# Kernel tuning notes

Measured on AMD Instinct MI355X. Metric: run time of the kernel, lower is better.

Reference implementation:

```python
import jax, jax.numpy as jnp
import numpy as np

B, S, H = 2, 2048, 2048
E, K = 8, 2            # num_local_experts, num_experts_per_tok
I, IS = 1024, 4096     # expert / shared-expert intermediate dims


def setup_inputs() -> dict:
    key = jax.random.key(0)
    ks = jax.random.split(key, 8)
    w = lambda k, shp: jax.random.normal(k, shp, dtype=jnp.float32) * 0.02
    return {
        "hidden_states": jax.random.normal(ks[0], (B, S, H), dtype=jnp.float32),
        "router_w": w(ks[1], (E, H)),
        "gate_w": w(ks[2], (E, I, H)),
        "up_w": w(ks[3], (E, I, H)),
        "down_w": w(ks[4], (E, H, I)),
        "shared_gate_w": w(ks[5], (IS, H)),
        "shared_up_w": w(ks[6], (IS, H)),
        "shared_down_w": w(ks[7], (H, IS)),
    }


def reference(hidden_states, router_w, gate_w, up_w, down_w,
              shared_gate_w, shared_up_w, shared_down_w):
    x = hidden_states  # [B,S,H]
    b, s, h = x.shape

    # Router: logits over experts, top-k, sigmoid of top values (computed in fp32)
    router_logits = jnp.einsum('bsh,eh->bse', x, router_w)           # [B,S,E]
    top_vals, top_idx = jax.lax.top_k(router_logits, K)              # [B,S,K]
    scores = jax.nn.sigmoid(top_vals.astype(jnp.float32)).astype(x.dtype)

    # Per-token per-expert input scale (each expert appears at most once in top-k)
    onehot = jax.nn.one_hot(top_idx, E, dtype=x.dtype)               # [B,S,K,E]
    scale = jnp.einsum('bsk,bske->bse', scores, onehot)              # [B,S,E]

    # Routed experts: scale is applied to the INPUT of each expert (as in the torch code).
    # With bias-free gated MLP, zero-scaled (unrouted) tokens produce exact zeros,
    # so the dense formulation matches the sparse gather/scatter exactly.
    xs = x.reshape(-1, h)                                            # [T,H]
    sc = scale.reshape(-1, E)                                        # [T,E]
    xe = xs[:, None, :] * sc[:, :, None]                             # [T,E,H]
    g = jnp.einsum('teh,eih->tei', xe, gate_w)                       # [T,E,I]
    u = jnp.einsum('teh,eih->tei', xe, up_w)                         # [T,E,I]
    hmid = jax.nn.silu(g) * u
    routed = jnp.einsum('tei,ehi->th', hmid, down_w).reshape(b, s, h)

    # Shared expert (dense gated MLP over all tokens)
    sg = jnp.einsum('bsh,ih->bsi', x, shared_gate_w)
    su = jnp.einsum('bsh,ih->bsi', x, shared_up_w)
    shared = jnp.einsum('bsi,hi->bsh', jax.nn.silu(sg) * su, shared_down_w)

    return routed + shared, router_logits
```

## Files before the change

kernel.cpp:

```cpp
#include <hip/hip_runtime.h>
#include <hip/hip_bf16.h>
#include <cstdint>
#include <cstddef>

typedef __bf16 bf16x8 __attribute__((ext_vector_type(8)));
typedef float  f32x4  __attribute__((ext_vector_type(4)));

static constexpr int TOK  = 4096;
static constexpr int H    = 2048;
static constexpr int E    = 8;
static constexpr int IDIM = 1024;
static constexpr int ISD  = 4096;
static constexpr int MAXTILES = 72;
static constexpr int MAXROWS  = MAXTILES * 128;


__device__ __forceinline__ void gll16(const void* g, void* l) {
  __builtin_amdgcn_global_load_lds((const __attribute__((address_space(1))) void*)g,
                                   (__attribute__((address_space(3))) void*)l, 16, 0, 0);
}

__device__ __forceinline__ unsigned short f2bf(float f) {
  unsigned int u = __float_as_uint(f);
  u = (u + 0x7fffu + ((u >> 16) & 1u)) >> 16;
  return (unsigned short)u;
}

__global__ __launch_bounds__(256) void detect_kernel(const unsigned int* __restrict__ x,
                                                     int* __restrict__ meta) {
  __shared__ int sh[256];
  const int tid = threadIdx.x;
  int c = 0;
  for (int i = tid; i < 1024; i += 256) {
    const unsigned int e = (x[i] >> 7) & 0xFFu;
    c += (e >= 100u && e <= 150u) ? 1 : 0;
  }
  sh[tid] = c;
  if (tid >= 4 && tid < 24) meta[tid] = 0;
  __syncthreads();
  if (tid == 0) {
    int s = 0;
    for (int i = 0; i < 256; ++i) s += sh[i];
    meta[0] = (s > 512) ? 1 : 0;
  }
}

__global__ __launch_bounds__(256) void convert_all_kernel(
    const float* __restrict__ s0, const float* __restrict__ s1,
    const float* __restrict__ s2, const float* __restrict__ s3,
    const float* __restrict__ s4, const float* __restrict__ s5,
    const float* __restrict__ s6, const float* __restrict__ s7,
    unsigned short* __restrict__ d0, unsigned short* __restrict__ d1,
    unsigned short* __restrict__ d2, unsigned short* __restrict__ d3,
    unsigned short* __restrict__ d4, unsigned short* __restrict__ d5,
    unsigned short* __restrict__ d6, unsigned short* __restrict__ d7,
    const int* __restrict__ flag)
{
  if (*flag) return;
  const int stride = gridDim.x * 256;
  const int base = blockIdx.x * 256 + threadIdx.x;
  auto go = [&](const float* s, unsigned short* d, int n4) {
    for (int i = base; i < n4; i += stride) {
      const float4 v = ((const float4*)s)[i];
      ushort4 o;
      o.x = f2bf(v.x); o.y = f2bf(v.y); o.z = f2bf(v.z); o.w = f2bf(v.w);
      ((ushort4*)d)[i] = o;
    }
  };
  go(s0, d0, (TOK * H) / 4);
  go(s1, d1, (E * H) / 4);
  go(s2, d2, (E * IDIM * H) / 4);
  go(s3, d3, (E * IDIM * H) / 4);
  go(s4, d4, (E * H * IDIM) / 4);
  go(s5, d5, (ISD * H) / 4);
  go(s6, d6, (ISD * H) / 4);
  go(s7, d7, (ISD * H) / 4);
}

__global__ __launch_bounds__(256) void router_kernel(
    const void* __restrict__ x_, const void* __restrict__ rw_,
    void* __restrict__ out, float* __restrict__ scale,
    int* __restrict__ meta, int* __restrict__ topk)
{
  const int bfmode = meta[0];
  const int t   = blockIdx.x;
  const int tid = threadIdx.x;
  const int l   = tid & 63, w = tid >> 6;
  const int off = tid * 8;

  float xs[8];
  if (bfmode) {
    bf16x8 v = *(const bf16x8*)((const unsigned short*)x_ + (size_t)t * H + off);
#pragma unroll
    for (int j = 0; j < 8; ++j) xs[j] = (float)v[j];
  } else {
    const float* xr = (const float*)x_ + (size_t)t * H + off;
    const float4 a = *(const float4*)xr;
    const float4 b = *(const float4*)(xr + 4);
    xs[0]=a.x; xs[1]=a.y; xs[2]=a.z; xs[3]=a.w; xs[4]=b.x; xs[5]=b.y; xs[6]=b.z; xs[7]=b.w;
  }

  float p[E];
#pragma unroll
  for (int e = 0; e < E; ++e) {
    float wv[8];
    if (bfmode) {
      bf16x8 v = *(const bf16x8*)((const unsigned short*)rw_ + (size_t)e * H + off);
#pragma unroll
      for (int j = 0; j < 8; ++j) wv[j] = (float)v[j];
    } else {
      const float* wr = (const float*)rw_ + (size_t)e * H + off;
      const float4 a = *(const float4*)wr;
      const float4 b = *(const float4*)(wr + 4);
      wv[0]=a.x; wv[1]=a.y; wv[2]=a.z; wv[3]=a.w; wv[4]=b.x; wv[5]=b.y; wv[6]=b.z; wv[7]=b.w;
    }
    float s = 0.f;
#pragma unroll
    for (int j = 0; j < 8; ++j) s = fmaf(xs[j], wv[j], s);
    p[e] = s;
  }
#pragma unroll
  for (int e = 0; e < E; ++e)
    for (int o = 32; o > 0; o >>= 1) p[e] += __shfl_down(p[e], o);

  __shared__ float red[E][4];
  __shared__ float lg[E];
  __shared__ float sres[2];
  __shared__ int   ires[2];
  if (l == 0) {
#pragma unroll
    for (int e = 0; e < E; ++e) red[e][w] = p[e];
  }
  __syncthreads();
  if (tid < E) {
    const float v = red[tid][0] + red[tid][1] + red[tid][2] + red[tid][3];
    lg[tid] = v;
    const size_t oi = (size_t)TOK * H + (size_t)t * E + tid;
    if (bfmode) ((unsigned short*)out)[oi] = f2bf(v);
    else        ((float*)out)[oi] = v;
  }
  __syncthreads();
  if (tid == 0) {
    int i0 = 0; float v0 = lg[0];
    for (int e = 1; e < E; ++e) if (lg[e] > v0) { v0 = lg[e]; i0 = e; }
    int i1 = -1; float v1 = 0.f; bool init = false;
    for (int e = 0; e < E; ++e) {
      if (e == i0) continue;
      if (!init || lg[e] > v1) { v1 = lg[e]; i1 = e; init = true; }
    }
    sres[0] = 1.f / (1.f + expf(-v0)); ires[0] = i0;
    sres[1] = 1.f / (1.f + expf(-v1)); ires[1] = i1;
    topk[2 * t + 0] = i0;
    topk[2 * t + 1] = i1;
    atomicAdd(&meta[4 + i0], 1);
    atomicAdd(&meta[4 + i1], 1);
  }
  __syncthreads();
  if (tid < E) {
    float s = 0.f;
    if (tid == ires[0]) s = sres[0];
    else if (tid == ires[1]) s = sres[1];
    scale[(size_t)t * E + tid] = s;
  }
}

__global__ __launch_bounds__(256) void scan_kernel(int* __restrict__ meta,
                                                   int* __restrict__ list) {
  const int tid = threadIdx.x;
  if (tid == 0) {
    int s = 0, nt = 0;
    for (int e = 0; e < E; ++e) {
      meta[24 + e] = s;
      const int cnt = meta[4 + e];
      const int tiles = (cnt + 127) >> 7;
      for (int i = 0; i < tiles; ++i) {
        meta[64 + nt]  = e;
        meta[136 + nt] = s + i * 128;
        ++nt;
      }
      s += tiles << 7;
    }
    meta[32] = s;
    meta[20] = nt;
  }
  for (int i = tid; i < MAXROWS; i += 256) list[i] = 0;
}

__global__ __launch_bounds__(256) void scatter_kernel(int* __restrict__ meta,
                                                      const int* __restrict__ topk,
                                                      int* __restrict__ list,
                                                      int* __restrict__ tokpos) {
  const int t = blockIdx.x * 256 + threadIdx.x;
  if (t >= TOK) return;
#pragma unroll
  for (int k = 0; k < 2; ++k) {
    const int e = topk[2 * t + k];
    const int p = atomicAdd(&meta[12 + e], 1);
    const int g = meta[24 + e] + p;
    list[g] = t;
    tokpos[2 * t + k] = g;
  }
}

#define GU_BAR_   __builtin_amdgcn_s_barrier()
#define GU_LGKM0_ { asm volatile("s_waitcnt lgkmcnt(0)" ::: "memory"); \
                    __builtin_amdgcn_sched_barrier(0); }
#define GU_VM4_   asm volatile("s_waitcnt vmcnt(4)" ::: "memory")
#define GU_VM0_   asm volatile("s_waitcnt vmcnt(0)" ::: "memory")

#define LDA_(p, mh) { _Pragma("unroll") for (int q2 = 0; q2 < 4; ++q2) { \
  _Pragma("unroll") for (int ks = 0; ks < 2; ++ks) { \
    const int row_ = 32 * (4 * (mh) + q2) + 16 * wm + lm; \
    a[q2][ks] = *(const bf16x8*)&ldsA[(p) * 16384 + row_ * 64 + \
                                      (((ks * 4 + quad) ^ (lm & 7)) * 8)]; } } }

#define LDB_(p, nh) { _Pragma("unroll") for (int nt2 = 0; nt2 < 2; ++nt2) { \
  _Pragma("unroll") for (int ks = 0; ks < 2; ++ks) { \
    const int row_ = 16 * (wn + 4 * (2 * (nh) + nt2)) + lm; \
    bb[nh][nt2][ks] = *(const bf16x8*)&ldsB[(p) * 16384 + row_ * 64 + \
                                            (((ks * 4 + quad) ^ (lm & 7)) * 8)]; } } }

#define MFMA_(mh, nh) { __builtin_amdgcn_s_setprio(1); \
  _Pragma("unroll") for (int q2 = 0; q2 < 4; ++q2) \
  _Pragma("unroll") for (int nt2 = 0; nt2 < 2; ++nt2) \
  _Pragma("unroll") for (int ks = 0; ks < 2; ++ks) \
    acc[4 * (mh) + q2][2 * (nh) + nt2] = __builtin_amdgcn_mfma_f32_16x16x32_bf16( \
      a[q2][ks], bb[nh][nt2][ks], acc[4 * (mh) + q2][2 * (nh) + nt2], 0, 0, 0); \
  __builtin_amdgcn_s_setprio(0); }

__global__ __launch_bounds__(512, 2) void gateup_shared_kernel(
    const void* __restrict__ xo_,  const unsigned short* __restrict__ cx,
    const void* __restrict__ sgo_, const unsigned short* __restrict__ csgw,
    const void* __restrict__ suo_, const unsigned short* __restrict__ csuw,
    unsigned short* __restrict__ hmid_sh, const int* __restrict__ meta)
{
  extern __shared__ unsigned short lds[];
  unsigned short* ldsA = lds;
  unsigned short* ldsB = lds + 32768;

  const int bfmode = meta[0];
  const unsigned short* x  = bfmode ? (const unsigned short*)xo_  : cx;
  const unsigned short* gw = bfmode ? (const unsigned short*)sgo_ : csgw;
  const unsigned short* uw = bfmode ? (const unsigned short*)suo_ : csuw;

  const int tid = threadIdx.x;
  const int l = tid & 63, w = tid >> 6;
  const int wm = w >> 2, wn = w & 3;
  const int quad = l >> 4, lm = l & 15;
  const int m0 = blockIdx.x * 256;
  const int jb = blockIdx.y * 128;

  const unsigned short* gB = gw + (size_t)jb * H;
  const unsigned short* uB = uw + (size_t)jb * H;

  const int sr0 = tid >> 3,         sc0 = tid & 7;
  const int sr1 = (tid + 512) >> 3, sc1 = (tid + 512) & 7;
  const int scc0 = sc0 ^ (sr0 & 7), scc1 = sc1 ^ (sr1 & 7);
  const int sd0 = tid * 8, sd1 = (tid + 512) * 8;

  auto stA = [&](int kt, int half) {
    unsigned short* d = ldsA + (kt & 1) * 16384 + half * 8192;
    const unsigned short* s = x + (size_t)(m0 + half * 128) * H + kt * 64;
    gll16(s + (size_t)sr0 * H + scc0 * 8, d + sd0);
    gll16(s + (size_t)sr1 * H + scc1 * 8, d + sd1);
  };
  auto stB = [&](int kt, int half) {
    unsigned short* d = ldsB + (kt & 1) * 16384 + half * 8192;
    const unsigned short* s = (half ? uB : gB) + kt * 64;
    gll16(s + (size_t)sr0 * H + scc0 * 8, d + sd0);
    gll16(s + (size_t)sr1 * H + scc1 * 8, d + sd1);
  };

  f32x4 acc[8][4] = {};
  bf16x8 a[4][2];
  bf16x8 bb[2][2][2];

  stA(0, 0); stB(0, 0); stB(0, 1); stA(0, 1);
  stB(1, 1); stA(1, 1);
  GU_VM4_; GU_BAR_;

  for (int i = 0; i < (H / 128) - 1; ++i) {
    const int t0 = 2 * i, t1 = 2 * i + 1;
    LDA_(0, 0); LDB_(0, 0); stA(t1, 0);
    GU_BAR_; GU_LGKM0_; MFMA_(0, 0); GU_BAR_;
    LDB_(0, 1); stB(t1, 0);
    GU_BAR_; GU_LGKM0_; MFMA_(0, 1); GU_BAR_;
    LDA_(0, 1); stA(t0 + 2, 0);
    GU_BAR_; GU_LGKM0_; MFMA_(1, 1); GU_BAR_;
    stB(t0 + 2, 0); GU_VM4_;
    GU_BAR_; GU_LGKM0_; MFMA_(1, 0); GU_BAR_;
    LDA_(1, 0); LDB_(1, 0); stB(t0 + 2, 1);
    GU_BAR_; GU_LGKM0_; MFMA_(0, 0); GU_BAR_;
    LDB_(1, 1); stA(t0 + 2, 1);
    GU_BAR_; GU_LGKM0_; MFMA_(0, 1); GU_BAR_;
    LDA_(1, 1); stB(t1 + 2, 1);
    GU_BAR_; GU_LGKM0_; MFMA_(1, 1); GU_BAR_;
    stA(t1 + 2, 1); GU_VM4_;
    GU_BAR_; GU_LGKM0_; MFMA_(1, 0); GU_BAR_;
  }

  {
    const int t1 = H / 64 - 1;
    LDA_(0, 0); LDB_(0, 0); stA(t1, 0);
    GU_BAR_; GU_LGKM0_; MFMA_(0, 0); GU_BAR_;
    LDB_(0, 1); stB(t1, 0);
    GU_BAR_; GU_LGKM0_; MFMA_(0, 1); GU_BAR_;
    LDA_(0, 1);
    GU_BAR_; GU_LGKM0_; MFMA_(1, 1); GU_BAR_;
    GU_VM0_;
    GU_BAR_; GU_LGKM0_; MFMA_(1, 0); GU_BAR_;
    LDA_(1, 0); LDB_(1, 0);
    GU_BAR_; GU_LGKM0_; MFMA_(0, 0); GU_BAR_;
    LDB_(1, 1);
    GU_BAR_; GU_LGKM0_; MFMA_(0, 1); GU_BAR_;
    LDA_(1, 1);
    GU_BAR_; GU_LGKM0_; MFMA_(1, 1); GU_BAR_;
    MFMA_(1, 0);
  }

#pragma unroll
  for (int mt = 0; mt < 8; ++mt) {
    const int trow = m0 + 32 * mt + 16 * wm + quad * 4;
#pragma unroll
    for (int ntp = 0; ntp < 2; ++ntp) {
      const int col = jb + wn * 16 + ntp * 64 + lm;
#pragma unroll
      for (int rr = 0; rr < 4; ++rr) {
        const float g = acc[mt][ntp][rr];
        const float u = acc[mt][ntp + 2][rr];
        const float hm = (g / (1.f + expf(-g))) * u;
        hmid_sh[(size_t)(trow + rr) * ISD + col] = f2bf(hm);
      }
    }
  }
}

__global__ __launch_bounds__(256) void gateup_routed_kernel(
    const void* __restrict__ xo_,  const unsigned short* __restrict__ cx,
    const void* __restrict__ gwo_, const unsigned short* __restrict__ cgw,
    const void* __restrict__ uwo_, const unsigned short* __restrict__ cuw,
    const float* __restrict__ scale, const int* __restrict__ list,
    unsigned short* __restrict__ hmid_r, const int* __restrict__ meta)
{
  if ((int)blockIdx.x >= meta[20]) return;
  const int bfmode = meta[0];
  const unsigned short* x      = bfmode ? (const unsigned short*)xo_  : cx;
  const unsigned short* gate_w = bfmode ? (const unsigned short*)gwo_ : cgw;
  const unsigned short* up_w   = bfmode ? (const unsigned short*)uwo_ : cuw;

  __shared__ __attribute__((aligned(16))) unsigned short As[128 * 64];
  __shared__ __attribute__((aligned(16))) unsigned short Bgs[64 * 64];
  __shared__ __attribute__((aligned(16))) unsigned short Bus[64 * 64];

  const int tid = threadIdx.x;
  const int l = tid & 63, w = tid >> 6;
  const int e    = meta[64 + blockIdx.x];
  const int base = meta[136 + blockIdx.x];
  const int jj   = blockIdx.y * 64;

  const unsigned short* gB = gate_w + ((size_t)e * IDIM + jj) * H;
  const unsigned short* uB = up_w   + ((size_t)e * IDIM + jj) * H;

  int tok[4];
#pragma unroll
  for (int j = 0; j < 4; ++j) tok[j] = list[base + ((j * 256 + tid) >> 3)];

  f32x4 accg[4][2] = {};
  f32x4 accu[4][2] = {};
  const int wm = (w >> 1) * 64;
  const int wn = (w & 1) * 32;
  const int quad = l >> 4, lm = l & 15;

  for (int k0 = 0; k0 < H; k0 += 64) {
#pragma unroll
    for (int j = 0; j < 4; ++j) {
      const int g = j * 256 + tid;
      const int r = g >> 3, c = g & 7;
      const int cc = c ^ (r & 7);
      gll16(x + (size_t)tok[j] * H + k0 + cc * 8, &As[g * 8]);
    }
#pragma unroll
    for (int j = 0; j < 2; ++j) {
      const int g = j * 256 + tid;
      const int r = g >> 3, c = g & 7;
      const int cc = c ^ (r & 7);
      gll16(gB + (size_t)r * H + k0 + cc * 8, &Bgs[g * 8]);
      gll16(uB + (size_t)r * H + k0 + cc * 8, &Bus[g * 8]);
    }
    __syncthreads();
#pragma unroll
    for (int ks = 0; ks < 64; ks += 32) {
      const int kc  = (ks >> 3) + quad;
      const int csw = (kc ^ (lm & 7)) * 8;
      bf16x8 a[4], bg[2], bu[2];
#pragma unroll
      for (int mt = 0; mt < 4; ++mt)
        a[mt] = *(const bf16x8*)&As[(wm + mt * 16 + lm) * 64 + csw];
#pragma unroll
      for (int nt = 0; nt < 2; ++nt) {
        bg[nt] = *(const bf16x8*)&Bgs[(wn + nt * 16 + lm) * 64 + csw];
        bu[nt] = *(const bf16x8*)&Bus[(wn + nt * 16 + lm) * 64 + csw];
      }
#pragma unroll
      for (int mt = 0; mt < 4; ++mt)
#pragma unroll
        for (int nt = 0; nt < 2; ++nt) {
          accg[mt][nt] = __builtin_amdgcn_mfma_f32_16x16x32_bf16(a[mt], bg[nt], accg[mt][nt], 0, 0, 0);
          accu[mt][nt] = __builtin_amdgcn_mfma_f32_16x16x32_bf16(a[mt], bu[nt], accu[mt][nt], 0, 0, 0);
        }
    }
    __syncthreads();
  }

#pragma unroll
  for (int mt = 0; mt < 4; ++mt) {
#pragma unroll
    for (int r = 0; r < 4; ++r) {
      const int row  = wm + mt * 16 + quad * 4 + r;
      const int gpos = base + row;
      const int token = list[gpos];
      const float s = scale[(size_t)token * E + e];
#pragma unroll
      for (int nt = 0; nt < 2; ++nt) {
        const int j = jj + wn + nt * 16 + lm;
        const float g = accg[mt][nt][r] * s;
        const float u = accu[mt][nt][r] * s;
        const float hm = (g / (1.f + expf(-g))) * u;
        hmid_r[(size_t)gpos * IDIM + j] = f2bf(hm);
      }
    }
  }
}

__global__ __launch_bounds__(256) void down_routed_kernel(
    const unsigned short* __restrict__ hmid_r,
    const void* __restrict__ dwo_, const unsigned short* __restrict__ cdw,
    float* __restrict__ dbuf, const int* __restrict__ meta)
{
  if ((int)blockIdx.y >= meta[20]) return;
  const int bfmode = meta[0];
  const unsigned short* down_w = bfmode ? (const unsigned short*)dwo_ : cdw;

  __shared__ __attribute__((aligned(16))) unsigned short As[128 * 64];
  __shared__ __attribute__((aligned(16))) unsigned short Bs[128 * 64];

  const int tid = threadIdx.x;
  const int l = tid & 63, w = tid >> 6;
  const int e    = meta[64 + blockIdx.y];
  const int base = meta[136 + blockIdx.y];
  const int n0 = blockIdx.x * 128;

  const unsigned short* Bbase = down_w + ((size_t)e * H + n0) * IDIM;

  f32x4 acc[4][4] = {};
  const int wm = (w >> 1) * 64;
  const int wn = (w & 1) * 64;
  const int quad = l >> 4, lm = l & 15;

  for (int k0 = 0; k0 < IDIM; k0 += 64) {
#pragma unroll
    for (int j = 0; j < 4; ++j) {
      const int g = j * 256 + tid;
      const int r = g >> 3, c = g & 7;
      const int cc = c ^ (r & 7);
      gll16(hmid_r + (size_t)(base + r) * IDIM + k0 + cc * 8, &As[g * 8]);
    }
#pragma unroll
    for (int j = 0; j < 4; ++j) {
      const int g = j * 256 + tid;
      const int r = g >> 3, c = g & 7;
      const int cc = c ^ (r & 7);
      gll16(Bbase + (size_t)r * IDIM + k0 + cc * 8, &Bs[g * 8]);
    }
    __syncthreads();
#pragma unroll
    for (int ks = 0; ks < 64; ks += 32) {
      const int kc  = (ks >> 3) + quad;
      const int csw = (kc ^ (lm & 7)) * 8;
      bf16x8 a[4], b[4];
#pragma unroll
      for (int mt = 0; mt < 4; ++mt)
        a[mt] = *(const bf16x8*)&As[(wm + mt * 16 + lm) * 64 + csw];
#pragma unroll
      for (int nt = 0; nt < 4; ++nt)
        b[nt] = *(const bf16x8*)&Bs[(wn + nt * 16 + lm) * 64 + csw];
#pragma unroll
      for (int mt = 0; mt < 4; ++mt)
#pragma unroll
        for (int nt = 0; nt < 4; ++nt)
          acc[mt][nt] = __builtin_amdgcn_mfma_f32_16x16x32_bf16(a[mt], b[nt], acc[mt][nt], 0, 0, 0);
    }
    __syncthreads();
  }

#pragma unroll
  for (int mt = 0; mt < 4; ++mt)
#pragma unroll
    for (int nt = 0; nt < 4; ++nt)
#pragma unroll
      for (int r = 0; r < 4; ++r) {
        const int row = wm + mt * 16 + quad * 4 + r;
        const int n   = n0 + wn + nt * 16 + lm;
        dbuf[(size_t)(base + row) * H + n] = acc[mt][nt][r];
      }
}

__global__ __launch_bounds__(256) void down_shared_kernel(
    const unsigned short* __restrict__ hmid_sh,
    const void* __restrict__ sdwo_, const unsigned short* __restrict__ csdw,
    const float* __restrict__ dbuf, const int* __restrict__ tokpos,
    void* __restrict__ out, const int* __restrict__ meta)
{
  const int bfmode = meta[0];
  const unsigned short* sdown_w = bfmode ? (const unsigned short*)sdwo_ : csdw;

  __shared__ __attribute__((aligned(16))) unsigned short As[128 * 64];
  __shared__ __attribute__((aligned(16))) unsigned short Bs[128 * 64];

  const int tid = threadIdx.x;
  const int l = tid & 63, w = tid >> 6;
  const int m0 = blockIdx.y * 128;
  const int n0 = blockIdx.x * 128;

  f32x4 acc[4][4] = {};
  const int wm = (w >> 1) * 64;
  const int wn = (w & 1) * 64;
  const int quad = l >> 4, lm = l & 15;

  for (int k0 = 0; k0 < ISD; k0 += 64) {
#pragma unroll
    for (int j = 0; j < 4; ++j) {
      const int g = j * 256 + tid;
      const int r = g >> 3, c = g & 7;
      const int cc = c ^ (r & 7);
      gll16(hmid_sh + (size_t)(m0 + r) * ISD + k0 + cc * 8, &As[g * 8]);
    }
#pragma unroll
    for (int j = 0; j < 4; ++j) {
      const int g = j * 256 + tid;
      const int r = g >> 3, c = g & 7;
      const int cc = c ^ (r & 7);
      gll16(sdown_w + (size_t)(n0 + r) * ISD + k0 + cc * 8, &Bs[g * 8]);
    }
    __syncthreads();
#pragma unroll
    for (int ks = 0; ks < 64; ks += 32) {
      const int kc  = (ks >> 3) + quad;
      const int csw = (kc ^ (lm & 7)) * 8;
      bf16x8 a[4], b[4];
#pragma unroll
      for (int mt = 0; mt < 4; ++mt)
        a[mt] = *(const bf16x8*)&As[(wm + mt * 16 + lm) * 64 + csw];
#pragma unroll
      for (int nt = 0; nt < 4; ++nt)
        b[nt] = *(const bf16x8*)&Bs[(wn + nt * 16 + lm) * 64 + csw];
#pragma unroll
      for (int mt = 0; mt < 4; ++mt)
#pragma unroll
        for (int nt = 0; nt < 4; ++nt)
          acc[mt][nt] = __builtin_amdgcn_mfma_f32_16x16x32_bf16(a[mt], b[nt], acc[mt][nt], 0, 0, 0);
    }
    __syncthreads();
  }

  if (bfmode) {
    unsigned short* o = (unsigned short*)out;
#pragma unroll
    for (int mt = 0; mt < 4; ++mt)
#pragma unroll
      for (int r = 0; r < 4; ++r) {
        const int t = m0 + wm + mt * 16 + quad * 4 + r;
        const int p0 = tokpos[2 * t], p1 = tokpos[2 * t + 1];
#pragma unroll
        for (int nt = 0; nt < 4; ++nt) {
          const int n = n0 + wn + nt * 16 + lm;
          const float v = acc[mt][nt][r]
                        + dbuf[(size_t)p0 * H + n] + dbuf[(size_t)p1 * H + n];
          o[(size_t)t * H + n] = f2bf(v);
        }
      }
  } else {
    float* o = (float*)out;
#pragma unroll
    for (int mt = 0; mt < 4; ++mt)
#pragma unroll
      for (int r = 0; r < 4; ++r) {
        const int t = m0 + wm + mt * 16 + quad * 4 + r;
        const int p0 = tokpos[2 * t], p1 = tokpos[2 * t + 1];
#pragma unroll
        for (int nt = 0; nt < 4; ++nt) {
          const int n = n0 + wn + nt * 16 + lm;
          o[(size_t)t * H + n] = acc[mt][nt][r]
                               + dbuf[(size_t)p0 * H + n] + dbuf[(size_t)p1 * H + n];
        }
      }
  }
}

extern "C" void kernel_launch(void* const* d_in, const int* in_sizes, int n_in,
                              void* d_out, int out_size, void* d_ws, size_t ws_size,
                              hipStream_t stream) {
  const void* x   = d_in[0];
  const void* rw  = d_in[1];
  const void* gw  = d_in[2];
  const void* uw  = d_in[3];
  const void* dw  = d_in[4];
  const void* sgw = d_in[5];
  const void* suw = d_in[6];
  const void* sdw = d_in[7];

  char* wsb = (char*)d_ws;
  int*   meta   = (int*)wsb;
  float* scale  = (float*)(wsb + 1024);
  int*   topk   = (int*)(wsb + 1024 + (size_t)TOK * E * 4);
  int*   list   = topk + (size_t)TOK * 2;
  int*   tokpos = list + MAXROWS;
  unsigned short* hmid_sh = (unsigned short*)(wsb + 234496);
  unsigned short* hmid_r  = hmid_sh + (size_t)TOK * ISD;
  unsigned short* cx   = hmid_r + (size_t)MAXROWS * IDIM;
  unsigned short* crw  = cx  + (size_t)TOK * H;
  unsigned short* cgw  = crw + (size_t)E * H;
  unsigned short* cuw  = cgw + (size_t)E * IDIM * H;
  unsigned short* cdw  = cuw + (size_t)E * IDIM * H;
  unsigned short* csgw = cdw + (size_t)E * H * IDIM;
  unsigned short* csuw = csgw + (size_t)ISD * H;
  unsigned short* csdw = csuw + (size_t)ISD * H;
  float* dbuf = (float*)cx;

  static int attr_set = 0;
  if (!attr_set) {
    hipFuncSetAttribute(reinterpret_cast<const void*>(gateup_shared_kernel),
                        hipFuncAttributeMaxDynamicSharedMemorySize, 131072);
    attr_set = 1;
  }

  detect_kernel<<<1, 256, 0, stream>>>((const unsigned int*)x, meta);

  convert_all_kernel<<<2048, 256, 0, stream>>>(
      (const float*)x, (const float*)rw, (const float*)gw, (const float*)uw,
      (const float*)dw, (const float*)sgw, (const float*)suw, (const float*)sdw,
      cx, crw, cgw, cuw, cdw, csgw, csuw, csdw, meta);

  router_kernel<<<TOK, 256, 0, stream>>>(x, rw, d_out, scale, meta, topk);
  scan_kernel<<<1, 256, 0, stream>>>(meta, list);
  scatter_kernel<<<TOK / 256, 256, 0, stream>>>(meta, topk, list, tokpos);

  dim3 g1(TOK / 256, ISD / 128);
  gateup_shared_kernel<<<g1, 512, 131072, stream>>>(x, cx, sgw, csgw, suw, csuw,
                                                    hmid_sh, meta);

  dim3 g2(MAXTILES, IDIM / 64);
  gateup_routed_kernel<<<g2, 256, 0, stream>>>(x, cx, gw, cgw, uw, cuw,
                                               scale, list, hmid_r, meta);

  dim3 g3(H / 128, MAXTILES);
  down_routed_kernel<<<g3, 256, 0, stream>>>(hmid_r, dw, cdw, dbuf, meta);

  dim3 g4(H / 128, TOK / 128);
  down_shared_kernel<<<g4, 256, 0, stream>>>(hmid_sh, sdw, csdw, dbuf, tokpos, d_out, meta);
}
```

Baseline: 898.7 us.

## Port routed gate/up GEMM to 256-row tiled pipelined kernel shared with dense path

The routed expert gate/up kernel is rewritten to reuse the shared expert's 512-thread, 256x128 tile, double-buffered LDS pipeline, now factored into a macro, with gathered token rows loaded via per-thread token indices. Expert segments are padded to multiples of 256 rows, and the scan emits both 256-row tiles for gate/up and 128-row subtiles for the down projection. This aims to raise MFMA utilisation and data reuse in the routed GEMM. The cost is more padding rows and a larger workspace layout.

```diff
diff --git a/kernel.cpp b/kernel.cpp
--- a/kernel.cpp
+++ b/kernel.cpp
@@ -11,8 +11,9 @@
 static constexpr int E    = 8;
 static constexpr int IDIM = 1024;
 static constexpr int ISD  = 4096;
-static constexpr int MAXTILES = 72;
-static constexpr int MAXROWS  = MAXTILES * 128;
+static constexpr int MAXT256 = 40;
+static constexpr int MAXT128 = 80;
+static constexpr int MAXROWS = MAXT256 * 256;
 
 
 __device__ __forceinline__ void gll16(const void* g, void* l) {
@@ -168,20 +169,23 @@
                                                    int* __restrict__ list) {
   const int tid = threadIdx.x;
   if (tid == 0) {
-    int s = 0, nt = 0;
+    int s = 0, n256 = 0, n128 = 0;
     for (int e = 0; e < E; ++e) {
       meta[24 + e] = s;
       const int cnt = meta[4 + e];
-      const int tiles = (cnt + 127) >> 7;
+      const int tiles = (cnt + 255) >> 8;
       for (int i = 0; i < tiles; ++i) {
-        meta[64 + nt]  = e;
-        meta[136 + nt] = s + i * 128;
-        ++nt;
+        meta[64 + n256]  = e;
+        meta[104 + n256] = s + i * 256;
+        ++n256;
+        meta[144 + n128] = e; meta[224 + n128] = s + i * 256;       ++n128;
+        meta[144 + n128] = e; meta[224 + n128] = s + i * 256 + 128; ++n128;
       }
-      s += tiles << 7;
+      s += tiles << 8;
     }
     meta[32] = s;
-    meta[20] = nt;
+    meta[20] = n256;
+    meta[21] = n128;
   }
   for (int i = tid; i < MAXROWS; i += 256) list[i] = 0;
 }
@@ -227,6 +231,48 @@
     acc[4 * (mh) + q2][2 * (nh) + nt2] = __builtin_amdgcn_mfma_f32_16x16x32_bf16( \
       a[q2][ks], bb[nh][nt2][ks], acc[4 * (mh) + q2][2 * (nh) + nt2], 0, 0, 0); \
   __builtin_amdgcn_s_setprio(0); }
+
+#define GU_PIPELINE_(STA, STB) \
+  STA(0, 0); STB(0, 0); STB(0, 1); STA(0, 1); \
+  STB(1, 1); STA(1, 1); \
+  GU_VM4_; GU_BAR_; \
+  for (int i = 0; i < (H / 128) - 1; ++i) { \
+    const int t0 = 2 * i, t1 = 2 * i + 1; \
+    LDA_(0, 0); LDB_(0, 0); STA(t1, 0); \
+    GU_BAR_; GU_LGKM0_; MFMA_(0, 0); GU_BAR_; \
+    LDB_(0, 1); STB(t1, 0); \
+    GU_BAR_; GU_LGKM0_; MFMA_(0, 1); GU_BAR_; \
+    LDA_(0, 1); STA(t0 + 2, 0); \
+    GU_BAR_; GU_LGKM0_; MFMA_(1, 1); GU_BAR_; \
+    STB(t0 + 2, 0); GU_VM4_; \
+    GU_BAR_; GU_LGKM0_; MFMA_(1, 0); GU_BAR_; \
+    LDA_(1, 0); LDB_(1, 0); STB(t0 + 2, 1); \
+    GU_BAR_; GU_LGKM0_; MFMA_(0, 0); GU_BAR_; \
+    LDB_(1, 1); STA(t0 + 2, 1); \
+    GU_BAR_; GU_LGKM0_; MFMA_(0, 1); GU_BAR_; \
+    LDA_(1, 1); STB(t1 + 2, 1); \
+    GU_BAR_; GU_LGKM0_; MFMA_(1, 1); GU_BAR_; \
+    STA(t1 + 2, 1); GU_VM4_; \
+    GU_BAR_; GU_LGKM0_; MFMA_(1, 0); GU_BAR_; \
+  } \
+  { \
+    const int t1 = H / 64 - 1; \
+    LDA_(0, 0); LDB_(0, 0); STA(t1, 0); \
+    GU_BAR_; GU_LGKM0_; MFMA_(0, 0); GU_BAR_; \
+    LDB_(0, 1); STB(t1, 0); \
+    GU_BAR_; GU_LGKM0_; MFMA_(0, 1); GU_BAR_; \
+    LDA_(0, 1); \
+    GU_BAR_; GU_LGKM0_; MFMA_(1, 1); GU_BAR_; \
+    GU_VM0_; \
+    GU_BAR_; GU_LGKM0_; MFMA_(1, 0); GU_BAR_; \
+    LDA_(1, 0); LDB_(1, 0); \
+    GU_BAR_; GU_LGKM0_; MFMA_(0, 0); GU_BAR_; \
+    LDB_(1, 1); \
+    GU_BAR_; GU_LGKM0_; MFMA_(0, 1); GU_BAR_; \
+    LDA_(1, 1); \
+    GU_BAR_; GU_LGKM0_; MFMA_(1, 1); GU_BAR_; \
+    MFMA_(1, 0); \
+  }
 
 __global__ __launch_bounds__(512, 2) void gateup_shared_kernel(
     const void* __restrict__ xo_,  const unsigned short* __restrict__ cx,
@@ -275,48 +321,7 @@
   bf16x8 a[4][2];
   bf16x8 bb[2][2][2];
 
-  stA(0, 0); stB(0, 0); stB(0, 1); stA(0, 1);
-  stB(1, 1); stA(1, 1);
-  GU_VM4_; GU_BAR_;
-
-  for (int i = 0; i < (H / 128) - 1; ++i) {
-    const int t0 = 2 * i, t1 = 2 * i + 1;
-    LDA_(0, 0); LDB_(0, 0); stA(t1, 0);
-    GU_BAR_; GU_LGKM0_; MFMA_(0, 0); GU_BAR_;
-    LDB_(0, 1); stB(t1, 0);
-    GU_BAR_; GU_LGKM0_; MFMA_(0, 1); GU_BAR_;
-    LDA_(0, 1); stA(t0 + 2, 0);
-    GU_BAR_; GU_LGKM0_; MFMA_(1, 1); GU_BAR_;
-    stB(t0 + 2, 0); GU_VM4_;
-    GU_BAR_; GU_LGKM0_; MFMA_(1, 0); GU_BAR_;
-    LDA_(1, 0); LDB_(1, 0); stB(t0 + 2, 1);
-    GU_BAR_; GU_LGKM0_; MFMA_(0, 0); GU_BAR_;
-    LDB_(1, 1); stA(t0 + 2, 1);
-    GU_BAR_; GU_LGKM0_; MFMA_(0, 1); GU_BAR_;
-    LDA_(1, 1); stB(t1 + 2, 1);
-    GU_BAR_; GU_LGKM0_; MFMA_(1, 1); GU_BAR_;
-    stA(t1 + 2, 1); GU_VM4_;
-    GU_BAR_; GU_LGKM0_; MFMA_(1, 0); GU_BAR_;
-  }
-
-  {
-    const int t1 = H / 64 - 1;
-    LDA_(0, 0); LDB_(0, 0); stA(t1, 0);
-    GU_BAR_; GU_LGKM0_; MFMA_(0, 0); GU_BAR_;
-    LDB_(0, 1); stB(t1, 0);
-    GU_BAR_; GU_LGKM0_; MFMA_(0, 1); GU_BAR_;
-    LDA_(0, 1);
-    GU_BAR_; GU_LGKM0_; MFMA_(1, 1); GU_BAR_;
-    GU_VM0_;
-    GU_BAR_; GU_LGKM0_; MFMA_(1, 0); GU_BAR_;
-    LDA_(1, 0); LDB_(1, 0);
-    GU_BAR_; GU_LGKM0_; MFMA_(0, 0); GU_BAR_;
-    LDB_(1, 1);
-    GU_BAR_; GU_LGKM0_; MFMA_(0, 1); GU_BAR_;
-    LDA_(1, 1);
-    GU_BAR_; GU_LGKM0_; MFMA_(1, 1); GU_BAR_;
-    MFMA_(1, 0);
-  }
+  GU_PIPELINE_(stA, stB);
 
 #pragma unroll
   for (int mt = 0; mt < 8; ++mt) {
@@ -335,7 +340,7 @@
   }
 }
 
-__global__ __launch_bounds__(256) void gateup_routed_kernel(
+__global__ __launch_bounds__(512, 2) void gateup_routed_kernel(
     const void* __restrict__ xo_,  const unsigned short* __restrict__ cx,
     const void* __restrict__ gwo_, const unsigned short* __restrict__ cgw,
     const void* __restrict__ uwo_, const unsigned short* __restrict__ cuw,
@@ -343,90 +348,70 @@
     unsigned short* __restrict__ hmid_r, const int* __restrict__ meta)
 {
   if ((int)blockIdx.x >= meta[20]) return;
+  extern __shared__ unsigned short lds[];
+  unsigned short* ldsA = lds;
+  unsigned short* ldsB = lds + 32768;
+
   const int bfmode = meta[0];
   const unsigned short* x      = bfmode ? (const unsigned short*)xo_  : cx;
   const unsigned short* gate_w = bfmode ? (const unsigned short*)gwo_ : cgw;
   const unsigned short* up_w   = bfmode ? (const unsigned short*)uwo_ : cuw;
 
-  __shared__ __attribute__((aligned(16))) unsigned short As[128 * 64];
-  __shared__ __attribute__((aligned(16))) unsigned short Bgs[64 * 64];
-  __shared__ __attribute__((aligned(16))) unsigned short Bus[64 * 64];
-
   const int tid = threadIdx.x;
   const int l = tid & 63, w = tid >> 6;
+  const int wm = w >> 2, wn = w & 3;
+  const int quad = l >> 4, lm = l & 15;
   const int e    = meta[64 + blockIdx.x];
-  const int base = meta[136 + blockIdx.x];
-  const int jj   = blockIdx.y * 64;
-
-  const unsigned short* gB = gate_w + ((size_t)e * IDIM + jj) * H;
-  const unsigned short* uB = up_w   + ((size_t)e * IDIM + jj) * H;
-
-  int tok[4];
-#pragma unroll
-  for (int j = 0; j < 4; ++j) tok[j] = list[base + ((j * 256 + tid) >> 3)];
-
-  f32x4 accg[4][2] = {};
-  f32x4 accu[4][2] = {};
-  const int wm = (w >> 1) * 64;
-  const int wn = (w & 1) * 32;
-  const int quad = l >> 4, lm = l & 15;
-
-  for (int k0 = 0; k0 < H; k0 += 64) {
-#pragma unroll
-    for (int j = 0; j < 4; ++j) {
-      const int g = j * 256 + tid;
-      const int r = g >> 3, c = g & 7;
-      const int cc = c ^ (r & 7);
-      gll16(x + (size_t)tok[j] * H + k0 + cc * 8, &As[g * 8]);
-    }
-#pragma unroll
-    for (int j = 0; j < 2; ++j) {
-      const int g = j * 256 + tid;
-      const int r = g >> 3, c = g & 7;
-      const int cc = c ^ (r & 7);
-      gll16(gB + (size_t)r * H + k0 + cc * 8, &Bgs[g * 8]);
-      gll16(uB + (size_t)r * H + k0 + cc * 8, &Bus[g * 8]);
-    }
-    __syncthreads();
-#pragma unroll
-    for (int ks = 0; ks < 64; ks += 32) {
-      const int kc  = (ks >> 3) + quad;
-      const int csw = (kc ^ (lm & 7)) * 8;
-      bf16x8 a[4], bg[2], bu[2];
-#pragma unroll
-      for (int mt = 0; mt < 4; ++mt)
-        a[mt] = *(const bf16x8*)&As[(wm + mt * 16 + lm) * 64 + csw];
-#pragma unroll
-      for (int nt = 0; nt < 2; ++nt) {
-        bg[nt] = *(const bf16x8*)&Bgs[(wn + nt * 16 + lm) * 64 + csw];
-        bu[nt] = *(const bf16x8*)&Bus[(wn + nt * 16 + lm) * 64 + csw];
-      }
-#pragma unroll
-      for (int mt = 0; mt < 4; ++mt)
-#pragma unroll
-        for (int nt = 0; nt < 2; ++nt) {
-          accg[mt][nt] = __builtin_amdgcn_mfma_f32_16x16x32_bf16(a[mt], bg[nt], accg[mt][nt], 0, 0, 0);
-          accu[mt][nt] = __builtin_amdgcn_mfma_f32_16x16x32_bf16(a[mt], bu[nt], accu[mt][nt], 0, 0, 0);
-        }
-    }
-    __syncthreads();
-  }
-
-#pragma unroll
-  for (int mt = 0; mt < 4; ++mt) {
-#pragma unroll
-    for (int r = 0; r < 4; ++r) {
-      const int row  = wm + mt * 16 + quad * 4 + r;
-      const int gpos = base + row;
-      const int token = list[gpos];
-      const float s = scale[(size_t)token * E + e];
-#pragma unroll
-      for (int nt = 0; nt < 2; ++nt) {
-        const int j = jj + wn + nt * 16 + lm;
-        const float g = accg[mt][nt][r] * s;
-        const float u = accu[mt][nt][r] * s;
+  const int base = meta[104 + blockIdx.x];
+  const int jb   = blockIdx.y * 128;
+
+  const unsigned short* gB = gate_w + ((size_t)e * IDIM + jb) * H;
+  const unsigned short* uB = up_w   + ((size_t)e * IDIM + jb) * H;
+
+  const int sr0 = tid >> 3,         sc0 = tid & 7;
+  const int sr1 = (tid + 512) >> 3, sc1 = (tid + 512) & 7;
+  const int scc0 = sc0 ^ (sr0 & 7), scc1 = sc1 ^ (sr1 & 7);
+  const int sd0 = tid * 8, sd1 = (tid + 512) * 8;
+
+  int tokh[2][2];
+#pragma unroll
+  for (int h = 0; h < 2; ++h) {
+    tokh[h][0] = list[base + h * 128 + sr0];
+    tokh[h][1] = list[base + h * 128 + sr1];
+  }
+
+  auto stA = [&](int kt, int half) {
+    unsigned short* d = ldsA + (kt & 1) * 16384 + half * 8192;
+    gll16(x + (size_t)tokh[half][0] * H + kt * 64 + scc0 * 8, d + sd0);
+    gll16(x + (size_t)tokh[half][1] * H + kt * 64 + scc1 * 8, d + sd1);
+  };
+  auto stB = [&](int kt, int half) {
+    unsigned short* d = ldsB + (kt & 1) * 16384 + half * 8192;
+    const unsigned short* s = (half ? uB : gB) + kt * 64;
+    gll16(s + (size_t)sr0 * H + scc0 * 8, d + sd0);
+    gll16(s + (size_t)sr1 * H + scc1 * 8, d + sd1);
+  };
+
+  f32x4 acc[8][4] = {};
+  bf16x8 a[4][2];
+  bf16x8 bb[2][2][2];
+
+  GU_PIPELINE_(stA, stB);
+
+#pragma unroll
+  for (int mt = 0; mt < 8; ++mt) {
+    const int rloc = 32 * mt + 16 * wm + quad * 4;
+#pragma unroll
+    for (int rr = 0; rr < 4; ++rr) {
+      const int gpos = base + rloc + rr;
+      const float s = scale[(size_t)list[gpos] * E + e];
+#pragma unroll
+      for (int ntp = 0; ntp < 2; ++ntp) {
+        const int col = jb + wn * 16 + ntp * 64 + lm;
+        const float g = acc[mt][ntp][rr] * s;
+        const float u = acc[mt][ntp + 2][rr] * s;
         const float hm = (g / (1.f + expf(-g))) * u;
-        hmid_r[(size_t)gpos * IDIM + j] = f2bf(hm);
+        hmid_r[(size_t)gpos * IDIM + col] = f2bf(hm);
       }
     }
   }
@@ -437,7 +422,7 @@
     const void* __restrict__ dwo_, const unsigned short* __restrict__ cdw,
     float* __restrict__ dbuf, const int* __restrict__ meta)
 {
-  if ((int)blockIdx.y >= meta[20]) return;
+  if ((int)blockIdx.y >= meta[21]) return;
   const int bfmode = meta[0];
   const unsigned short* down_w = bfmode ? (const unsigned short*)dwo_ : cdw;
 
@@ -446,8 +431,8 @@
 
   const int tid = threadIdx.x;
   const int l = tid & 63, w = tid >> 6;
-  const int e    = meta[64 + blockIdx.y];
-  const int base = meta[136 + blockIdx.y];
+  const int e    = meta[144 + blockIdx.y];
+  const int base = meta[224 + blockIdx.y];
   const int n0 = blockIdx.x * 128;
 
   const unsigned short* Bbase = down_w + ((size_t)e * H + n0) * IDIM;
@@ -611,11 +596,11 @@
 
   char* wsb = (char*)d_ws;
   int*   meta   = (int*)wsb;
-  float* scale  = (float*)(wsb + 1024);
-  int*   topk   = (int*)(wsb + 1024 + (size_t)TOK * E * 4);
+  float* scale  = (float*)(wsb + 2048);
+  int*   topk   = (int*)(wsb + 2048 + (size_t)TOK * E * 4);
   int*   list   = topk + (size_t)TOK * 2;
   int*   tokpos = list + MAXROWS;
-  unsigned short* hmid_sh = (unsigned short*)(wsb + 234496);
+  unsigned short* hmid_sh = (unsigned short*)(wsb + 262144);
   unsigned short* hmid_r  = hmid_sh + (size_t)TOK * ISD;
   unsigned short* cx   = hmid_r + (size_t)MAXROWS * IDIM;
   unsigned short* crw  = cx  + (size_t)TOK * H;
@@ -631,6 +616,8 @@
   if (!attr_set) {
     hipFuncSetAttribute(reinterpret_cast<const void*>(gateup_shared_kernel),
                         hipFuncAttributeMaxDynamicSharedMemorySize, 131072);
+    hipFuncSetAttribute(reinterpret_cast<const void*>(gateup_routed_kernel),
+                        hipFuncAttributeMaxDynamicSharedMemorySize, 131072);
     attr_set = 1;
   }
 
@@ -649,11 +636,11 @@
   gateup_shared_kernel<<<g1, 512, 131072, stream>>>(x, cx, sgw, csgw, suw, csuw,
                                                     hmid_sh, meta);
 
-  dim3 g2(MAXTILES, IDIM / 64);
-  gateup_routed_kernel<<<g2, 256, 0, stream>>>(x, cx, gw, cgw, uw, cuw,
-                                               scale, list, hmid_r, meta);
-
-  dim3 g3(H / 128, MAXTILES);
+  dim3 g2(MAXT256, IDIM / 128);
+  gateup_routed_kernel<<<g2, 512, 131072, stream>>>(x, cx, gw, cgw, uw, cuw,
+                                                    scale, list, hmid_r, meta);
+
+  dim3 g3(H / 128, MAXT128);
   down_routed_kernel<<<g3, 256, 0, stream>>>(hmid_r, dw, cdw, dbuf, meta);
 
   dim3 g4(H / 128, TOK / 128);
```

Measured after the change: 865.9 us. 1.04x faster.
